# Kernel optimization log

Hardware: AMD Instinct MI355X
Metric: run time of the kernel (lower is better)

Reference implementation:

```python
import jax, jax.numpy as jnp
import numpy as np
import math

B, S, D, H = 4, 1024, 1024, 16
DK = D // H
DF = 4 * D
SPARSITY = 0.3
EPS = 1e-5

def _ln(x, g, b):
    mu = jnp.mean(x, axis=-1, keepdims=True)
    var = jnp.mean((x - mu) ** 2, axis=-1, keepdims=True)
    return (x - mu) * jax.lax.rsqrt(var + EPS) * g + b

def setup_inputs() -> dict:
    key = jax.random.key(0)
    ks = jax.random.split(key, 8)
    sc = 0.02
    return {
        "x": jax.random.normal(ks[0], (B, S, D), jnp.float32),
        "Wq": jax.random.normal(ks[1], (D, D), jnp.float32) * sc,
        "bq": jnp.zeros((D,), jnp.float32),
        "Wk": jax.random.normal(ks[2], (D, D), jnp.float32) * sc,
        "bk": jnp.zeros((D,), jnp.float32),
        "Wv": jax.random.normal(ks[3], (D, D), jnp.float32) * sc,
        "bv": jnp.zeros((D,), jnp.float32),
        "Wo": jax.random.normal(ks[4], (D, D), jnp.float32) * sc,
        "bo": jnp.zeros((D,), jnp.float32),
        "W1": jax.random.normal(ks[5], (DF, D), jnp.float32) * sc,
        "b1": jnp.zeros((DF,), jnp.float32),
        "Wm": jax.random.normal(ks[6], (DF, DF), jnp.float32) * sc,
        "bm": jnp.zeros((DF,), jnp.float32),
        "W2": jax.random.normal(ks[7], (D, DF), jnp.float32) * sc,
        "b2": jnp.zeros((D,), jnp.float32),
        "g1": jnp.ones((D,), jnp.float32),
        "be1": jnp.zeros((D,), jnp.float32),
        "g2": jnp.ones((D,), jnp.float32),
        "be2": jnp.zeros((D,), jnp.float32),
    }

def reference(x, Wq, bq, Wk, bk, Wv, bv, Wo, bo, W1, b1, Wm, bm, W2, b2, g1, be1, g2, be2):
    h = _ln(x, g1, be1)
    def heads(W, b):
        return (h @ W.T + b).reshape(B, S, H, DK).transpose(0, 2, 1, 3)  # [B,H,S,DK]
    Q, K, V = heads(Wq, bq), heads(Wk, bk), heads(Wv, bv)
    scores = jnp.einsum("bhqd,bhkd->bhqk", Q, K) / math.sqrt(DK)  # [B,H,S,S]
    k = max(1, int(S * SPARSITY))
    vals, idx = jax.lax.top_k(scores, k)  # [B,H,S,k]
    # scatter top-k values into a -inf canvas (faithful to torch scatter_)
    N = B * H * S
    rows = jnp.arange(N)[:, None]
    mask2 = jnp.full((N, S), -jnp.inf, scores.dtype)
    mask2 = mask2.at[rows, idx.reshape(N, k)].set(vals.reshape(N, k))
    attn = jax.nn.softmax(mask2.reshape(B, H, S, S), axis=-1)
    out = jnp.einsum("bhqk,bhkd->bhqd", attn, V)
    out = out.transpose(0, 2, 1, 3).reshape(B, S, D) @ Wo.T + bo
    x = x + out
    h2 = _ln(x, g2, be2)
    f = jax.nn.gelu(h2 @ W1.T + b1, approximate=False)
    f = jax.nn.gelu(f @ Wm.T + bm, approximate=False)
    f = f @ W2.T + b2
    x = x + f
    return x, attn
```

## Files before the change

kernel.cpp:

```cpp
#include <hip/hip_runtime.h>
#include <hip/hip_bf16.h>

typedef __hip_bfloat16 bf16;
typedef float v4f __attribute__((ext_vector_type(4)));
typedef short v8s __attribute__((ext_vector_type(8)));

#define KSEL 307

__device__ static inline void async16(bf16* lds, const bf16* g) {
    __builtin_amdgcn_global_load_lds(
        (const __attribute__((address_space(1))) void*)g,
        (__attribute__((address_space(3))) void*)lds, 16, 0, 0);
}

__device__ static inline unsigned short f2bu(float f) {
    __hip_bfloat16 h = __float2bfloat16(f);
    return *reinterpret_cast<unsigned short*>(&h);
}

__device__ static inline unsigned pk2(float a, float b) {
    __hip_bfloat162 h = __float22bfloat162_rn(make_float2(a, b));
    return *reinterpret_cast<unsigned*>(&h);
}

__device__ static inline float gelu_f(float v) {
    float c = v * fmaf(v * v, 0.0356774081f, 0.7978845608f);
    return v / (1.0f + __expf(-2.0f * c));
}

struct F2BP { const float* src[7]; bf16* dst[7]; int n4[7]; };

__global__ void __launch_bounds__(256) f2b_multi(F2BP p) {
    int s = blockIdx.y;
    const float* __restrict__ in = p.src[s];
    bf16* __restrict__ out = p.dst[s];
    int n4 = p.n4[s];
    for (int i = blockIdx.x * 256 + threadIdx.x; i < n4; i += gridDim.x * 256) {
        float4 v = ((const float4*)in)[i];
        ushort4 u = make_ushort4(f2bu(v.x), f2bu(v.y), f2bu(v.z), f2bu(v.w));
        ((ushort4*)out)[i] = u;
    }
}

__global__ void __launch_bounds__(256) ln_kernel(const float* __restrict__ x,
                                                 const float* __restrict__ g,
                                                 const float* __restrict__ be,
                                                 bf16* __restrict__ out) {
    int row = blockIdx.x;
    int tid = threadIdx.x;
    const float* xr = x + row * 1024;
    float4 v = ((const float4*)xr)[tid];
    float s = v.x + v.y + v.z + v.w;
    float s2 = v.x*v.x + v.y*v.y + v.z*v.z + v.w*v.w;
    for (int off = 32; off > 0; off >>= 1) {
        s  += __shfl_down(s, off);
        s2 += __shfl_down(s2, off);
    }
    __shared__ float sh[4], sh2[4];
    int w = tid >> 6;
    if ((tid & 63) == 0) { sh[w] = s; sh2[w] = s2; }
    __syncthreads();
    float mean = (sh[0]+sh[1]+sh[2]+sh[3]) * (1.0f / 1024.f);
    float ms   = (sh2[0]+sh2[1]+sh2[2]+sh2[3]) * (1.0f / 1024.f);
    float var  = ms - mean*mean;
    float rs   = rsqrtf(var + 1e-5f);
    float4 gg = ((const float4*)g)[tid];
    float4 bb = ((const float4*)be)[tid];
    ushort4 o = make_ushort4(
        f2bu((v.x-mean)*rs*gg.x + bb.x),
        f2bu((v.y-mean)*rs*gg.y + bb.y),
        f2bu((v.z-mean)*rs*gg.z + bb.z),
        f2bu((v.w-mean)*rs*gg.w + bb.w));
    ((ushort4*)out)[row * 256 + tid] = o;
}

__global__ void __launch_bounds__(256) topk_softmax(float* __restrict__ sc) {
    __shared__ int hist[4][256];
    const int tid = threadIdx.x;
    const int wid = tid >> 6, lane = tid & 63;
    float* p = sc + ((long long)blockIdx.x * 4 + wid) * 1024;
    int* h = hist[wid];

    float v[16];
    unsigned key[16];
#pragma unroll
    for (int j = 0; j < 4; ++j) {
        float4 t = *(const float4*)(p + lane * 4 + j * 256);
        v[j*4+0] = t.x; v[j*4+1] = t.y; v[j*4+2] = t.z; v[j*4+3] = t.w;
    }
#pragma unroll
    for (int j = 0; j < 16; ++j) {
        unsigned u = __float_as_uint(v[j]);
        key[j] = (u & 0x80000000u) ? ~u : (u | 0x80000000u);
    }

    unsigned prefix = 0;
    int need = KSEL;
#pragma unroll
    for (int pass = 0; pass < 2; ++pass) {
        const int shift = 24 - 8 * pass;
        *(int4*)&h[lane * 4] = make_int4(0, 0, 0, 0);
        asm volatile("s_waitcnt lgkmcnt(0)" ::: "memory");
#pragma unroll
        for (int j = 0; j < 16; ++j) {
            bool cand = (pass == 0) || ((key[j] >> 24) == prefix);
            if (cand) atomicAdd(&h[(key[j] >> shift) & 255], 1);
        }
        asm volatile("s_waitcnt lgkmcnt(0)" ::: "memory");
        int4 hc = *(const int4*)&h[lane * 4];
        int s_local = hc.x + hc.y + hc.z + hc.w;
        int sfx = s_local;
#pragma unroll
        for (int off = 1; off < 64; off <<= 1) {
            int o = __shfl_down(sfx, off);
            if (lane + off < 64) sfx += o;
        }
        int sfx_next = __shfl_down(sfx, 1);
        if (lane == 63) sfx_next = 0;
        int above_lane = sfx - s_local;
        int suf3 = above_lane + hc.w;
        int suf2 = suf3 + hc.z;
        int suf1 = suf2 + hc.y;
        int suf0 = suf1 + hc.x;
        int bloc = -1, abv = 0;
        if (suf0 >= need && suf1 < need)     { bloc = lane*4+0; abv = suf1; }
        if (suf1 >= need && suf2 < need)     { bloc = lane*4+1; abv = suf2; }
        if (suf2 >= need && suf3 < need)     { bloc = lane*4+2; abv = suf3; }
        if (suf3 >= need && sfx_next < need) { bloc = lane*4+3; abv = sfx_next; }
        unsigned long long mask = __ballot(bloc >= 0);
        int src = __ffsll((unsigned long long)mask) - 1;
        int b = __shfl(bloc, src);
        int above = __shfl(abv, src);
        prefix = (prefix << 8) | (unsigned)b;
        need -= above;
    }

    float mx = v[0];
#pragma unroll
    for (int j = 1; j < 16; ++j) mx = fmaxf(mx, v[j]);
#pragma unroll
    for (int off = 32; off > 0; off >>= 1) mx = fmaxf(mx, __shfl_xor(mx, off));
    float sum = 0.f;
#pragma unroll
    for (int j = 0; j < 16; ++j) {
        bool sel = (key[j] >> 16) >= prefix;
        v[j] = sel ? __expf(v[j] - mx) : 0.f;
        sum += v[j];
    }
#pragma unroll
    for (int off = 32; off > 0; off >>= 1) sum += __shfl_xor(sum, off);
    float inv = 1.0f / sum;
#pragma unroll
    for (int j = 0; j < 4; ++j) {
        float4 o;
        o.x = v[j*4+0]*inv; o.y = v[j*4+1]*inv; o.z = v[j*4+2]*inv; o.w = v[j*4+3]*inv;
        *(float4*)(p + lane * 4 + j * 256) = o;
    }
}

template<int K, int LDA, int LDB, int LDC, int N, int BMODE, int ACT, int BM>
__global__ void __launch_bounds__(256) gemm_t(const bf16* __restrict__ A,
                                              const bf16* __restrict__ B,
                                              float* __restrict__ Cf,
                                              bf16* __restrict__ Cb,
                                              const float* __restrict__ bias,
                                              const float* __restrict__ resid,
                                              float scale) {
    __shared__ __align__(16) bf16 As[128 * 32];
    __shared__ __align__(16) bf16 Bs[128 * 32];
    int offA = 0, offB = 0, offC = 0;
    if (BM == 1) {
        int z = blockIdx.z;
        int b = z >> 4, h = z & 15;
        offA = b * 1048576 + h * 64;
        offB = offA;
        offC = z * 1048576;
    }
    const int tid = threadIdx.x;
    const int w = tid >> 6, lane = tid & 63;
    const int tm = blockIdx.y * 128, tn = blockIdx.x * 128;
    const int q = lane >> 4, m16 = lane & 15;
    const int r0 = (w >> 1) * 64, c0 = (w & 1) * 64;
    const int srow = lane >> 2, scol = (lane & 3) * 8;

    v4f acc[4][4];
#pragma unroll
    for (int i = 0; i < 4; ++i)
#pragma unroll
        for (int j = 0; j < 4; ++j) acc[i][j] = (v4f){0.f, 0.f, 0.f, 0.f};

    const bf16* Ab = A + offA + (tm + w * 16 + srow) * LDA + scol;
    const bf16* Bb = B + offB + (tn + w * 16 + srow) * LDB + scol;
    bf16* Asw = &As[(w * 16) * 32];
    bf16* Bsw = &Bs[(w * 16) * 32];

#pragma unroll 1
    for (int k0 = 0; k0 < K; k0 += 32) {
        async16(Asw,           Ab + k0);
        async16(Asw + 64 * 32, Ab + 64 * LDA + k0);
        async16(Bsw,           Bb + k0);
        async16(Bsw + 64 * 32, Bb + 64 * LDB + k0);
        __syncthreads();
        v8s af[4], bfr[4];
#pragma unroll
        for (int i = 0; i < 4; ++i)
            af[i] = *(const v8s*)&As[(r0 + 16 * i + m16) * 32 + q * 8];
#pragma unroll
        for (int j = 0; j < 4; ++j)
            bfr[j] = *(const v8s*)&Bs[(c0 + 16 * j + m16) * 32 + q * 8];
#pragma unroll
        for (int i = 0; i < 4; ++i)
#pragma unroll
            for (int j = 0; j < 4; ++j)
                acc[i][j] = __builtin_amdgcn_mfma_f32_16x16x32_bf16(af[i], bfr[j], acc[i][j], 0, 0, 0);
        __syncthreads();
    }

    float bc[4];
#pragma unroll
    for (int j = 0; j < 4; ++j)
        bc[j] = (BMODE == 1) ? bias[tn + c0 + 16 * j + m16] : 0.f;

#pragma unroll
    for (int i = 0; i < 4; ++i) {
#pragma unroll
        for (int r = 0; r < 4; ++r) {
            int row = tm + r0 + 16 * i + q * 4 + r;
            float br = (BMODE == 2) ? bias[row] : 0.f;
            int rowbase = offC + row * LDC + tn + c0 + m16;
#pragma unroll
            for (int j = 0; j < 4; ++j) {
                float v = acc[i][j][r] * scale + bc[j] + br;
                if (ACT) v = gelu_f(v);
                int idx = rowbase + 16 * j;
                if (resid) v += resid[idx];
                if (Cf) Cf[idx] = v;
                if (Cb) Cb[idx] = __float2bfloat16(v);
            }
        }
    }
}

template<int K, int LDA, int LDB, int LDC>
__global__ void __launch_bounds__(512, 2) gemm256(const bf16* __restrict__ A,
                                                  const bf16* __restrict__ B,
                                                  bf16* __restrict__ C,
                                                  const float* __restrict__ bias) {
    __shared__ __align__(16) bf16 As[4][256 * 32];
    __shared__ __align__(16) bf16 Bs[4][256 * 32];

    constexpr int nt = K / 32;
    static_assert(nt >= 4 && (nt % 4) == 0, "K must be multiple of 128");

    const int tid = threadIdx.x;
    const int w = tid >> 6, lane = tid & 63;
    const int wm = w >> 2, wn = w & 3;
    const int q = lane >> 4, m16 = lane & 15;

    int bid = blockIdx.y * 16 + blockIdx.x;
    int xcd = bid & 7, inner = bid >> 3;
    int by = (xcd & 3) * 4 + (inner & 3);
    int bx = (xcd >> 2) * 8 + (inner >> 2);
    const int tm = by * 256, tn = bx * 256;

    const int srow = lane >> 2;
    const int scol = (lane & 3) * 8;
    const bf16* Ag = A + (tm + w * 32 + srow) * LDA + scol;
    const bf16* Bg = B + (tn + w * 32 + srow) * LDB + scol;

    v4f acc[8][4];
#pragma unroll
    for (int i = 0; i < 8; ++i)
#pragma unroll
        for (int j = 0; j < 4; ++j) acc[i][j] = (v4f){0.f, 0.f, 0.f, 0.f};

    const int aoff = (wm * 128 + m16) * 32 + q * 8;
    const int boff = (wn * 64 + m16) * 32 + q * 8;

#pragma unroll
    for (int t = 0; t < 2; ++t) {
        async16(&As[t][(w * 32) * 32],      Ag + t * 32);
        async16(&As[t][(w * 32 + 16) * 32], Ag + 16 * LDA + t * 32);
        async16(&Bs[t][(w * 32) * 32],      Bg + t * 32);
        async16(&Bs[t][(w * 32 + 16) * 32], Bg + 16 * LDB + t * 32);
    }
    asm volatile("s_waitcnt vmcnt(4)" ::: "memory");
    __builtin_amdgcn_s_barrier();
    __builtin_amdgcn_sched_barrier(0);

#pragma unroll 1
    for (int t4 = 0; t4 < nt; t4 += 4) {
#pragma unroll
        for (int tt = 0; tt < 4; ++tt) {
            const int t = t4 + tt;
            const int cur = tt;
            const int pre = (tt + 2) & 3;
            int kt = t + 2; if (kt >= nt) kt = 0;
            const bf16* Asrc = Ag + kt * 32;
            const bf16* Bsrc = Bg + kt * 32;

            v8s af[4], bfr[4];
#pragma unroll
            for (int i = 0; i < 4; ++i)
                af[i] = *(const v8s*)&As[cur][aoff + i * 512];
#pragma unroll
            for (int j = 0; j < 4; ++j)
                bfr[j] = *(const v8s*)&Bs[cur][boff + j * 512];
            async16(&As[pre][(w * 32) * 32],      Asrc);
            async16(&As[pre][(w * 32 + 16) * 32], Asrc + 16 * LDA);
            __builtin_amdgcn_s_barrier();
            asm volatile("s_waitcnt lgkmcnt(0)" ::: "memory");
            __builtin_amdgcn_sched_barrier(0);
            __builtin_amdgcn_s_setprio(1);
#pragma unroll
            for (int i = 0; i < 4; ++i)
#pragma unroll
                for (int j = 0; j < 4; ++j)
                    acc[i][j] = __builtin_amdgcn_mfma_f32_16x16x32_bf16(af[i], bfr[j], acc[i][j], 0, 0, 0);
            __builtin_amdgcn_s_setprio(0);
            __builtin_amdgcn_sched_barrier(0);
            __builtin_amdgcn_s_barrier();
            __builtin_amdgcn_sched_barrier(0);

            v8s af2[4];
#pragma unroll
            for (int i = 0; i < 4; ++i)
                af2[i] = *(const v8s*)&As[cur][aoff + 2048 + i * 512];
            async16(&Bs[pre][(w * 32) * 32],      Bsrc);
            async16(&Bs[pre][(w * 32 + 16) * 32], Bsrc + 16 * LDB);
            __builtin_amdgcn_s_barrier();
            asm volatile("s_waitcnt lgkmcnt(0)" ::: "memory");
            __builtin_amdgcn_sched_barrier(0);
            __builtin_amdgcn_s_setprio(1);
#pragma unroll
            for (int i = 0; i < 4; ++i)
#pragma unroll
                for (int j = 0; j < 4; ++j)
                    acc[i + 4][j] = __builtin_amdgcn_mfma_f32_16x16x32_bf16(af2[i], bfr[j], acc[i + 4][j], 0, 0, 0);
            __builtin_amdgcn_s_setprio(0);
            asm volatile("s_waitcnt vmcnt(4)" ::: "memory");
            __builtin_amdgcn_sched_barrier(0);
            __builtin_amdgcn_s_barrier();
            __builtin_amdgcn_sched_barrier(0);
        }
    }

    float bc[4];
#pragma unroll
    for (int j = 0; j < 4; ++j)
        bc[j] = bias[tn + wn * 64 + 16 * j + m16];

#pragma unroll
    for (int i = 0; i < 8; ++i) {
#pragma unroll
        for (int r = 0; r < 4; ++r) {
            int row = tm + wm * 128 + 16 * i + q * 4 + r;
            int rowbase = row * LDC + tn + wn * 64 + m16;
#pragma unroll
            for (int j = 0; j < 4; ++j) {
                float v = acc[i][j][r] + bc[j];
                v = gelu_f(v);
                C[rowbase + 16 * j] = __float2bfloat16(v);
            }
        }
    }
}

__global__ void __launch_bounds__(256) attnv_kernel(const float* __restrict__ P,
                                                    const bf16* __restrict__ VT,
                                                    bf16* __restrict__ out) {
    __shared__ __align__(16) bf16 As[128 * 32];
    __shared__ __align__(16) bf16 Bs[64 * 32];
    int z = blockIdx.z, b = z >> 4, h = z & 15;
    int tid = threadIdx.x, w = tid >> 6, lane = tid & 63;
    int q = lane >> 4, m16 = lane & 15;
    int srow = lane >> 2, scol = (lane & 3) * 8;

    const float* Ab = P + z * 1048576 + (blockIdx.y * 128 + (tid >> 1)) * 1024 + (tid & 1) * 16;
    const bf16* Bb = VT + (h * 64 + w * 16 + srow) * 4096 + b * 1024 + scol;
    uint4* asd = (uint4*)&As[(tid >> 1) * 32 + (tid & 1) * 16];
    bf16* bsw = &Bs[(w * 16) * 32];

    v4f acc[2][4];
#pragma unroll
    for (int i = 0; i < 2; ++i)
#pragma unroll
        for (int j = 0; j < 4; ++j) acc[i][j] = (v4f){0.f, 0.f, 0.f, 0.f};

#pragma unroll 1
    for (int k0 = 0; k0 < 1024; k0 += 32) {
        const float4* s4 = (const float4*)(Ab + k0);
        float4 f0 = s4[0], f1 = s4[1], f2 = s4[2], f3 = s4[3];
        async16(bsw, Bb + k0);
        uint4 u0, u1;
        u0.x = pk2(f0.x, f0.y); u0.y = pk2(f0.z, f0.w);
        u0.z = pk2(f1.x, f1.y); u0.w = pk2(f1.z, f1.w);
        u1.x = pk2(f2.x, f2.y); u1.y = pk2(f2.z, f2.w);
        u1.z = pk2(f3.x, f3.y); u1.w = pk2(f3.z, f3.w);
        asd[0] = u0; asd[1] = u1;
        __syncthreads();
        v8s af[2], bfr[4];
        af[0] = *(const v8s*)&As[(w * 32 + m16) * 32 + q * 8];
        af[1] = *(const v8s*)&As[(w * 32 + 16 + m16) * 32 + q * 8];
#pragma unroll
        for (int j = 0; j < 4; ++j)
            bfr[j] = *(const v8s*)&Bs[(16 * j + m16) * 32 + q * 8];
#pragma unroll
        for (int i = 0; i < 2; ++i)
#pragma unroll
            for (int j = 0; j < 4; ++j)
                acc[i][j] = __builtin_amdgcn_mfma_f32_16x16x32_bf16(af[i], bfr[j], acc[i][j], 0, 0, 0);
        __syncthreads();
    }

    int orow0 = b * 1024 + blockIdx.y * 128 + w * 32;
#pragma unroll
    for (int i = 0; i < 2; ++i)
#pragma unroll
        for (int r = 0; r < 4; ++r) {
            int row = orow0 + 16 * i + q * 4 + r;
#pragma unroll
            for (int j = 0; j < 4; ++j) {
                int col = h * 64 + 16 * j + m16;
                out[row * 1024 + col] = __float2bfloat16(acc[i][j][r]);
            }
        }
}

extern "C" void kernel_launch(void* const* d_in, const int* in_sizes, int n_in,
                              void* d_out, int out_size, void* d_ws, size_t ws_size,
                              hipStream_t stream) {
    (void)in_sizes; (void)n_in; (void)out_size; (void)ws_size;
    const float* x  = (const float*)d_in[0];
    const float* Wq = (const float*)d_in[1];
    const float* bq = (const float*)d_in[2];
    const float* Wk = (const float*)d_in[3];
    const float* bk = (const float*)d_in[4];
    const float* Wv = (const float*)d_in[5];
    const float* bv = (const float*)d_in[6];
    const float* Wo = (const float*)d_in[7];
    const float* bo = (const float*)d_in[8];
    const float* W1 = (const float*)d_in[9];
    const float* b1 = (const float*)d_in[10];
    const float* Wm = (const float*)d_in[11];
    const float* bm = (const float*)d_in[12];
    const float* W2 = (const float*)d_in[13];
    const float* b2 = (const float*)d_in[14];
    const float* g1 = (const float*)d_in[15];
    const float* be1 = (const float*)d_in[16];
    const float* g2 = (const float*)d_in[17];
    const float* be2 = (const float*)d_in[18];

    char* ws = (char*)d_ws;
    const size_t MB = 1024 * 1024;
    bf16* WQb = (bf16*)(ws + 0 * MB);
    bf16* WKb = (bf16*)(ws + 2 * MB);
    bf16* WVb = (bf16*)(ws + 4 * MB);
    bf16* WOb = (bf16*)(ws + 6 * MB);
    bf16* W1b = (bf16*)(ws + 8 * MB);
    bf16* WMb = (bf16*)(ws + 16 * MB);
    bf16* W2b = (bf16*)(ws + 48 * MB);
    bf16* HB  = (bf16*)(ws + 56 * MB);
    bf16* QB  = (bf16*)(ws + 64 * MB);
    bf16* KB  = (bf16*)(ws + 72 * MB);
    bf16* VT  = (bf16*)(ws + 80 * MB);
    bf16* AT  = (bf16*)(ws + 88 * MB);
    float* X1 = (float*)(ws + 96 * MB);
    bf16* F1  = (bf16*)(ws + 112 * MB);
    bf16* F2  = (bf16*)(ws + 144 * MB);

    float* out_x  = (float*)d_out;
    float* scores = out_x + 4194304;

    F2BP fp;
    fp.src[0] = Wq; fp.dst[0] = WQb; fp.n4[0] = 262144;
    fp.src[1] = Wk; fp.dst[1] = WKb; fp.n4[1] = 262144;
    fp.src[2] = Wv; fp.dst[2] = WVb; fp.n4[2] = 262144;
    fp.src[3] = Wo; fp.dst[3] = WOb; fp.n4[3] = 262144;
    fp.src[4] = W1; fp.dst[4] = W1b; fp.n4[4] = 1048576;
    fp.src[5] = Wm; fp.dst[5] = WMb; fp.n4[5] = 4194304;
    fp.src[6] = W2; fp.dst[6] = W2b; fp.n4[6] = 1048576;
    hipLaunchKernelGGL(f2b_multi, dim3(1024, 7), dim3(256), 0, stream, fp);

    hipLaunchKernelGGL(ln_kernel, dim3(4096), dim3(256), 0, stream, x, g1, be1, HB);

    gemm_t<1024,1024,1024,1024,1024,1,0,0><<<dim3(8,32,1), 256, 0, stream>>>(
        HB, WQb, nullptr, QB, bq, nullptr, 1.f);
    gemm_t<1024,1024,1024,1024,1024,1,0,0><<<dim3(8,32,1), 256, 0, stream>>>(
        HB, WKb, nullptr, KB, bk, nullptr, 1.f);
    gemm_t<1024,1024,1024,4096,4096,2,0,0><<<dim3(32,8,1), 256, 0, stream>>>(
        WVb, HB, nullptr, VT, bv, nullptr, 1.f);

    gemm_t<64,1024,1024,1024,1024,0,0,1><<<dim3(8,8,64), 256, 0, stream>>>(
        QB, KB, scores, nullptr, nullptr, nullptr, 0.125f);

    hipLaunchKernelGGL(topk_softmax, dim3(16384), dim3(256), 0, stream, scores);

    hipLaunchKernelGGL(attnv_kernel, dim3(1,8,64), dim3(256), 0, stream, scores, VT, AT);

    gemm_t<1024,1024,1024,1024,1024,1,0,0><<<dim3(8,32,1), 256, 0, stream>>>(
        AT, WOb, X1, nullptr, bo, x, 1.f);

    hipLaunchKernelGGL(ln_kernel, dim3(4096), dim3(256), 0, stream, X1, g2, be2, HB);

    gemm256<1024,1024,1024,4096><<<dim3(16,16,1), 512, 0, stream>>>(HB, W1b, F1, b1);
    gemm256<4096,4096,4096,4096><<<dim3(16,16,1), 512, 0, stream>>>(F1, WMb, F2, bm);

    gemm_t<4096,4096,4096,1024,1024,1,0,0><<<dim3(8,32,1), 256, 0, stream>>>(
        F2, W2b, out_x, nullptr, b2, X1, 1.f);
}
```

Before: 1.080 ms.

## Store attention scores as bf16 intermediate and swizzle GEMM LDS tiles

The QK^T GEMM now writes scores as bf16 into a workspace buffer instead of fp32 into the output. The top-k/softmax kernel reads those bf16 values, runs the radix select on 16-bit keys, and writes fp32 probabilities to the output. This halves the traffic for the score write and re-read. Separately, both GEMM kernels XOR-swizzle the 8-element column chunks in LDS, on the global source side and the fragment read side, to reduce bank conflicts. Rounding scores to bf16 before selection can change which elements make the top-k on near-ties, and it lowers softmax precision.

After: 1.058 ms. 2.1% less time.

```diff
diff --git a/kernel.cpp b/kernel.cpp
--- a/kernel.cpp
+++ b/kernel.cpp
@@ -74,36 +74,41 @@
     ((ushort4*)out)[row * 256 + tid] = o;
 }
 
-__global__ void __launch_bounds__(256) topk_softmax(float* __restrict__ sc) {
+__global__ void __launch_bounds__(256) topk_softmax(const unsigned short* __restrict__ scb,
+                                                    float* __restrict__ out) {
     __shared__ int hist[4][256];
     const int tid = threadIdx.x;
     const int wid = tid >> 6, lane = tid & 63;
-    float* p = sc + ((long long)blockIdx.x * 4 + wid) * 1024;
+    const long long row = (long long)blockIdx.x * 4 + wid;
+    const unsigned short* pb = scb + row * 1024;
+    float* po = out + row * 1024;
     int* h = hist[wid];
 
+    unsigned short raw[16];
+    unsigned key[16];
     float v[16];
-    unsigned key[16];
 #pragma unroll
     for (int j = 0; j < 4; ++j) {
-        float4 t = *(const float4*)(p + lane * 4 + j * 256);
-        v[j*4+0] = t.x; v[j*4+1] = t.y; v[j*4+2] = t.z; v[j*4+3] = t.w;
+        ushort4 t = *(const ushort4*)(pb + lane * 4 + j * 256);
+        raw[j*4+0] = t.x; raw[j*4+1] = t.y; raw[j*4+2] = t.z; raw[j*4+3] = t.w;
     }
 #pragma unroll
     for (int j = 0; j < 16; ++j) {
-        unsigned u = __float_as_uint(v[j]);
-        key[j] = (u & 0x80000000u) ? ~u : (u | 0x80000000u);
+        unsigned u = raw[j];
+        key[j] = (u & 0x8000u) ? (0xFFFFu & ~u) : (u | 0x8000u);
+        v[j] = __uint_as_float(u << 16);
     }
 
     unsigned prefix = 0;
     int need = KSEL;
 #pragma unroll
     for (int pass = 0; pass < 2; ++pass) {
-        const int shift = 24 - 8 * pass;
+        const int shift = 8 - 8 * pass;
         *(int4*)&h[lane * 4] = make_int4(0, 0, 0, 0);
         asm volatile("s_waitcnt lgkmcnt(0)" ::: "memory");
 #pragma unroll
         for (int j = 0; j < 16; ++j) {
-            bool cand = (pass == 0) || ((key[j] >> 24) == prefix);
+            bool cand = (pass == 0) || ((key[j] >> 8) == prefix);
             if (cand) atomicAdd(&h[(key[j] >> shift) & 255], 1);
         }
         asm volatile("s_waitcnt lgkmcnt(0)" ::: "memory");
@@ -143,7 +148,7 @@
     float sum = 0.f;
 #pragma unroll
     for (int j = 0; j < 16; ++j) {
-        bool sel = (key[j] >> 16) >= prefix;
+        bool sel = key[j] >= prefix;
         v[j] = sel ? __expf(v[j] - mx) : 0.f;
         sum += v[j];
     }
@@ -154,7 +159,7 @@
     for (int j = 0; j < 4; ++j) {
         float4 o;
         o.x = v[j*4+0]*inv; o.y = v[j*4+1]*inv; o.z = v[j*4+2]*inv; o.w = v[j*4+3]*inv;
-        *(float4*)(p + lane * 4 + j * 256) = o;
+        *(float4*)(po + lane * 4 + j * 256) = o;
     }
 }
 
@@ -181,7 +186,9 @@
     const int tm = blockIdx.y * 128, tn = blockIdx.x * 128;
     const int q = lane >> 4, m16 = lane & 15;
     const int r0 = (w >> 1) * 64, c0 = (w & 1) * 64;
-    const int srow = lane >> 2, scol = (lane & 3) * 8;
+    const int srow = lane >> 2;
+    const int scol = ((lane & 3) ^ ((lane >> 3) & 3)) * 8;
+    const int sq = q ^ ((m16 >> 1) & 3);
 
     v4f acc[4][4];
 #pragma unroll
@@ -204,10 +211,10 @@
         v8s af[4], bfr[4];
 #pragma unroll
         for (int i = 0; i < 4; ++i)
-            af[i] = *(const v8s*)&As[(r0 + 16 * i + m16) * 32 + q * 8];
+            af[i] = *(const v8s*)&As[(r0 + 16 * i + m16) * 32 + sq * 8];
 #pragma unroll
         for (int j = 0; j < 4; ++j)
-            bfr[j] = *(const v8s*)&Bs[(c0 + 16 * j + m16) * 32 + q * 8];
+            bfr[j] = *(const v8s*)&Bs[(c0 + 16 * j + m16) * 32 + sq * 8];
 #pragma unroll
         for (int i = 0; i < 4; ++i)
 #pragma unroll
@@ -264,7 +271,7 @@
     const int tm = by * 256, tn = bx * 256;
 
     const int srow = lane >> 2;
-    const int scol = (lane & 3) * 8;
+    const int scol = ((lane & 3) ^ ((lane >> 3) & 3)) * 8;
     const bf16* Ag = A + (tm + w * 32 + srow) * LDA + scol;
     const bf16* Bg = B + (tn + w * 32 + srow) * LDB + scol;
 
@@ -274,8 +281,9 @@
 #pragma unroll
         for (int j = 0; j < 4; ++j) acc[i][j] = (v4f){0.f, 0.f, 0.f, 0.f};
 
-    const int aoff = (wm * 128 + m16) * 32 + q * 8;
-    const int boff = (wn * 64 + m16) * 32 + q * 8;
+    const int sq = q ^ ((m16 >> 1) & 3);
+    const int aoff = (wm * 128 + m16) * 32 + sq * 8;
+    const int boff = (wn * 64 + m16) * 32 + sq * 8;
 
 #pragma unroll
     for (int t = 0; t < 2; ++t) {
@@ -468,6 +476,7 @@
     float* X1 = (float*)(ws + 96 * MB);
     bf16* F1  = (bf16*)(ws + 112 * MB);
     bf16* F2  = (bf16*)(ws + 144 * MB);
+    bf16* SCb = (bf16*)(ws + 96 * MB);
 
     float* out_x  = (float*)d_out;
     float* scores = out_x + 4194304;
@@ -492,9 +501,10 @@
         WVb, HB, nullptr, VT, bv, nullptr, 1.f);
 
     gemm_t<64,1024,1024,1024,1024,0,0,1><<<dim3(8,8,64), 256, 0, stream>>>(
-        QB, KB, scores, nullptr, nullptr, nullptr, 0.125f);
-
-    hipLaunchKernelGGL(topk_softmax, dim3(16384), dim3(256), 0, stream, scores);
+        QB, KB, nullptr, SCb, nullptr, nullptr, 0.125f);
+
+    hipLaunchKernelGGL(topk_softmax, dim3(16384), dim3(256), 0, stream,
+                       (const unsigned short*)SCb, scores);
 
     hipLaunchKernelGGL(attnv_kernel, dim3(1,8,64), dim3(256), 0, stream, scores, VT, AT);
 
```
